# Kernel tuning notes

Measured on AMD Instinct MI355X. Metric: run time of the kernel, lower is better.

Reference implementation:

```python
import jax, jax.numpy as jnp
import numpy as np

F = 8          # number of tables/features
B = 4096       # batch size (number of bags per feature)
V = 100000     # rows per embedding table
D = 128        # embedding dim
N = 81920      # total jagged values per feature (avg bag length ~20)


def setup_inputs() -> dict:
    key = jax.random.key(0)
    k_vals, k_offs, k_tab = jax.random.split(key, 3)
    # jagged indices into each table: [F, N]
    values = jax.random.randint(k_vals, (F, N), 0, V, dtype=jnp.int32)
    # offsets with include_last_offset=True: [F, B+1], nondecreasing, offs[0]=0, offs[-1]=N
    inner = jnp.sort(jax.random.randint(k_offs, (F, B - 1), 0, N + 1, dtype=jnp.int32), axis=1)
    offsets = jnp.concatenate(
        [jnp.zeros((F, 1), jnp.int32), inner, jnp.full((F, 1), N, jnp.int32)], axis=1
    )
    # embedding tables: [F, V, D]
    tables = jax.random.normal(k_tab, (F, V, D), dtype=jnp.float32)
    return {"values": values, "offsets": offsets, "tables": tables}


def reference(values, offsets, tables):
    """EmbeddingBagCollection forward: per-feature EmbeddingBag(sum) + concat.

    values:  [F, N] int32 indices
    offsets: [F, B+1] int32 (include_last_offset)
    tables:  [F, V, D] float32
    returns: [B, F*D] pooled embeddings (KeyedTensor.values())
    """
    pos = jnp.arange(N)

    def per_feature(vals, offs, table):
        # bag id for each value: index of the bag whose [offs[i], offs[i+1]) contains pos
        seg = jnp.searchsorted(offs, pos, side="right") - 1  # [N] in [0, B-1]
        gathered = table[vals]                               # [N, D]
        return jax.ops.segment_sum(gathered, seg, num_segments=B)  # [B, D]

    pooled = jax.vmap(per_feature)(values, offsets, tables)  # [F, B, D]
    return jnp.transpose(pooled, (1, 0, 2)).reshape(B, F * D)
```

## Files before the change

### kernel.cpp

```cpp
#include <hip/hip_runtime.h>

#define FF 8
#define BB 4096
#define VV 100000
#define DD 128
#define NN 81920

__global__ __launch_bounds__(256, 8) void ebc_pool_kernel(
    const int* __restrict__ values,
    const int* __restrict__ offsets,
    const float* __restrict__ tables,
    float* __restrict__ out)
{
    const int wave = threadIdx.x >> 6;
    const int lane = threadIdx.x & 63;

    const int f = blockIdx.x & 7;
    const int b = ((blockIdx.x >> 3) << 2) + wave;

    const int* __restrict__ offs = offsets + f * (BB + 1);
    const int start = __builtin_amdgcn_readfirstlane(offs[b]);
    const int end   = __builtin_amdgcn_readfirstlane(offs[b + 1]);

    const int* __restrict__ vals = values + f * NN;
    const float* __restrict__ tab = tables + (size_t)f * (VV * DD);

    float ax = 0.f, ay = 0.f;

    for (int i0 = start; i0 < end; i0 += 64) {
        int g = i0 + lane;
        g = (g < end) ? g : (end - 1);
        const int idxv = vals[g];

        const int rem = end - i0;
        const int nr = (rem < 64) ? rem : 64;

        for (int r = 0; r < nr; r += 8) {
#define EBC_ROW(k)                                                          \
            const int   in##k = (r + k) < nr;                               \
            const int   rr##k = in##k ? (r + k) : 0;                        \
            const float w##k  = in##k ? 1.f : 0.f;                          \
            const int   s##k  = __builtin_amdgcn_readlane(idxv, rr##k);     \
            const float2 v##k = *((const float2*)(tab + (size_t)s##k * DD) + lane);
            EBC_ROW(0) EBC_ROW(1) EBC_ROW(2) EBC_ROW(3)
            EBC_ROW(4) EBC_ROW(5) EBC_ROW(6) EBC_ROW(7)
#undef EBC_ROW
            ax += ((w0 * v0.x + w1 * v1.x) + (w2 * v2.x + w3 * v3.x)) +
                  ((w4 * v4.x + w5 * v5.x) + (w6 * v6.x + w7 * v7.x));
            ay += ((w0 * v0.y + w1 * v1.y) + (w2 * v2.y + w3 * v3.y)) +
                  ((w4 * v4.y + w5 * v5.y) + (w6 * v6.y + w7 * v7.y));
        }
    }

    float2* __restrict__ o = (float2*)(out + (size_t)b * (FF * DD) + f * DD);
    o[lane] = make_float2(ax, ay);
}

extern "C" void kernel_launch(void* const* d_in, const int* in_sizes, int n_in,
                              void* d_out, int out_size, void* d_ws, size_t ws_size,
                              hipStream_t stream) {
    const int*   values  = (const int*)d_in[0];
    const int*   offsets = (const int*)d_in[1];
    const float* tables  = (const float*)d_in[2];
    float*       out     = (float*)d_out;

    const int total_bags = FF * BB;
    const int blocks = total_bags / 4;
    ebc_pool_kernel<<<blocks, 256, 0, stream>>>(values, offsets, tables, out);
}
```

Baseline: 526.7 us.

## Split wave into half-waves loading float4 rows for two bag entries at once

Each wave now processes two embedding rows per load step, with each half-wave fetching a full 512-byte row as float4 per lane instead of float2. The row index comes from a per-lane shuffle rather than a uniform readlane, and the two halves are reduced with a cross-half shuffle before a single float4 store. Launch bounds drop to 4 waves per SIMD to leave room for more registers. The aim is wider memory transactions and more rows in flight per wave, traded against lower occupancy and non-uniform (VGPR) addressing.

Result: faster. 508.2 us, median of 2 (-3.5%).

```diff
diff --git a/kernel.cpp b/kernel.cpp
--- a/kernel.cpp
+++ b/kernel.cpp
@@ -6,7 +6,7 @@
 #define DD 128
 #define NN 81920
 
-__global__ __launch_bounds__(256, 8) void ebc_pool_kernel(
+__global__ __launch_bounds__(256, 4) void ebc_pool_kernel(
     const int* __restrict__ values,
     const int* __restrict__ offsets,
     const float* __restrict__ tables,
@@ -14,6 +14,8 @@
 {
     const int wave = threadIdx.x >> 6;
     const int lane = threadIdx.x & 63;
+    const int half = lane >> 5;
+    const int hl   = lane & 31;
 
     const int f = blockIdx.x & 7;
     const int b = ((blockIdx.x >> 3) << 2) + wave;
@@ -25,35 +27,51 @@
     const int* __restrict__ vals = values + f * NN;
     const float* __restrict__ tab = tables + (size_t)f * (VV * DD);
 
-    float ax = 0.f, ay = 0.f;
+    float4 acc0 = make_float4(0.f, 0.f, 0.f, 0.f);
+    float4 acc1 = make_float4(0.f, 0.f, 0.f, 0.f);
 
-    for (int i0 = start; i0 < end; i0 += 64) {
-        int g = i0 + lane;
+    for (int c0 = start; c0 < end; c0 += 64) {
+        int g = c0 + lane;
         g = (g < end) ? g : (end - 1);
         const int idxv = vals[g];
 
-        const int rem = end - i0;
-        const int nr = (rem < 64) ? rem : 64;
+        const int rem = end - c0;
+        const int nch = (rem < 64) ? rem : 64;
 
-        for (int r = 0; r < nr; r += 8) {
-#define EBC_ROW(k)                                                          \
-            const int   in##k = (r + k) < nr;                               \
-            const int   rr##k = in##k ? (r + k) : 0;                        \
-            const float w##k  = in##k ? 1.f : 0.f;                          \
-            const int   s##k  = __builtin_amdgcn_readlane(idxv, rr##k);     \
-            const float2 v##k = *((const float2*)(tab + (size_t)s##k * DD) + lane);
+        for (int r = 0; r < nch; r += 16) {
+#define EBC_ROW(k)                                                           \
+            const int   rr##k = r + 2 * (k) + half;                          \
+            const int   ok##k = rr##k < nch;                                 \
+            const int   rc##k = ok##k ? rr##k : 0;                           \
+            const int   id##k = __shfl(idxv, rc##k, 64);                     \
+            const float w##k  = ok##k ? 1.f : 0.f;                           \
+            const float4 v##k = ((const float4*)(tab + (size_t)id##k * DD))[hl];
             EBC_ROW(0) EBC_ROW(1) EBC_ROW(2) EBC_ROW(3)
             EBC_ROW(4) EBC_ROW(5) EBC_ROW(6) EBC_ROW(7)
 #undef EBC_ROW
-            ax += ((w0 * v0.x + w1 * v1.x) + (w2 * v2.x + w3 * v3.x)) +
-                  ((w4 * v4.x + w5 * v5.x) + (w6 * v6.x + w7 * v7.x));
-            ay += ((w0 * v0.y + w1 * v1.y) + (w2 * v2.y + w3 * v3.y)) +
-                  ((w4 * v4.y + w5 * v5.y) + (w6 * v6.y + w7 * v7.y));
+            acc0.x += (w0 * v0.x + w1 * v1.x) + (w2 * v2.x + w3 * v3.x);
+            acc0.y += (w0 * v0.y + w1 * v1.y) + (w2 * v2.y + w3 * v3.y);
+            acc0.z += (w0 * v0.z + w1 * v1.z) + (w2 * v2.z + w3 * v3.z);
+            acc0.w += (w0 * v0.w + w1 * v1.w) + (w2 * v2.w + w3 * v3.w);
+            acc1.x += (w4 * v4.x + w5 * v5.x) + (w6 * v6.x + w7 * v7.x);
+            acc1.y += (w4 * v4.y + w5 * v5.y) + (w6 * v6.y + w7 * v7.y);
+            acc1.z += (w4 * v4.z + w5 * v5.z) + (w6 * v6.z + w7 * v7.z);
+            acc1.w += (w4 * v4.w + w5 * v5.w) + (w6 * v6.w + w7 * v7.w);
         }
     }
 
-    float2* __restrict__ o = (float2*)(out + (size_t)b * (FF * DD) + f * DD);
-    o[lane] = make_float2(ax, ay);
+    acc0.x += acc1.x; acc0.y += acc1.y; acc0.z += acc1.z; acc0.w += acc1.w;
+
+    acc0.x += __shfl_xor(acc0.x, 32, 64);
+    acc0.y += __shfl_xor(acc0.y, 32, 64);
+    acc0.z += __shfl_xor(acc0.z, 32, 64);
+    acc0.w += __shfl_xor(acc0.w, 32, 64);
+
+    if (half == 0) {
+        float4* __restrict__ o =
+            (float4*)(out + (size_t)b * (FF * DD) + f * DD);
+        o[hl] = acc0;
+    }
 }
 
 extern "C" void kernel_launch(void* const* d_in, const int* in_sizes, int n_in,
```
